# Performance work log

Measured on AMD Instinct MI355X. Metric: run time of the kernel, lower is better.

## Reference

```python
import jax, jax.numpy as jnp
import numpy as np

BATCH = 4096
IN_CAPS = 64
OUT_CAPS = 16
IN_DIM = 64
OUT_DIM = 64
NUM_ITER = 3
LN_EPS = 1e-5


def setup_inputs() -> dict:
    key = jax.random.key(0)
    ks = jax.random.split(key, 13)
    n = lambda k, s: jax.random.normal(k, s, dtype=jnp.float32)
    return {
        "x_inp": n(ks[0], (BATCH, IN_CAPS, IN_DIM)),
        "W_A": n(ks[1], (IN_CAPS, IN_DIM)),
        "B_A": n(ks[2], (IN_CAPS,)),
        "W_F1": n(ks[3], (IN_CAPS, IN_DIM, IN_DIM)),
        "W_F2": n(ks[4], (OUT_CAPS, IN_DIM, OUT_DIM)),
        "B_F2": n(ks[5], (OUT_CAPS, OUT_DIM)),
        "W_G1": n(ks[6], (OUT_DIM, OUT_DIM)),
        "W_G2": n(ks[7], (OUT_CAPS, OUT_DIM, IN_DIM)),
        "B_G2": n(ks[8], (OUT_CAPS, IN_DIM)),
        "ln_gamma": jnp.ones((OUT_DIM,), jnp.float32),
        "ln_beta": jnp.zeros((OUT_DIM,), jnp.float32),
        "W_S": n(ks[9], (IN_CAPS, OUT_CAPS, IN_DIM)),
        "B_S": n(ks[10], (IN_CAPS, OUT_CAPS)),
        "beta_use": n(ks[11], (IN_CAPS, OUT_CAPS)),
        "beta_ign": n(ks[12], (IN_CAPS, OUT_CAPS)),
    }


def _layer_norm(x, gamma, beta):
    mu = jnp.mean(x, axis=-1, keepdims=True)
    var = jnp.var(x, axis=-1, keepdims=True)  # biased, matches torch LayerNorm
    return (x - mu) * jax.lax.rsqrt(var + LN_EPS) * gamma + beta


def reference(x_inp, W_A, B_A, W_F1, W_F2, B_F2, W_G1, W_G2, B_G2,
              ln_gamma, ln_beta, W_S, B_S, beta_use, beta_ign):
    B = x_inp.shape[0]
    inv_sqrt = np.float32(1.0 / np.sqrt(IN_DIM))
    # activation logits per input capsule: [B, in_caps]
    a_e = jnp.einsum('bif,if->bi', x_inp, W_A) * inv_sqrt + B_A
    f_a_e = jax.nn.sigmoid(a_e)  # loop-invariant
    # temp_F is loop-invariant: [B, in_caps, in_dim]
    temp_F = jnp.einsum('bif,ifh->bih', x_inp, W_F1) * inv_sqrt
    R_em = jnp.full((B, IN_CAPS, OUT_CAPS), 1.0 / OUT_CAPS, dtype=x_inp.dtype)
    x_out = None
    for _ in range(NUM_ITER):
        D_use = f_a_e[:, :, None] * R_em                      # [B,i,m]
        D_ign = f_a_e[:, :, None] - D_use                     # [B,i,m]
        phi_em = beta_use * D_use - beta_ign * D_ign          # [B,i,m]
        temp_F_routed = phi_em.sum(axis=-1)[:, :, None] * temp_F  # [B,i,h]
        x_out = jnp.einsum('bih,mhd->bmd', temp_F_routed, W_F2) + B_F2  # [B,m,d]
        x_out_norm = _layer_norm(x_out, ln_gamma, ln_beta)
        temp_G = jnp.einsum('bmd,dh->bmh', x_out_norm, W_G1)  # [B,m,d]
        x_inp_hat = jnp.einsum('bmh,mhi->bmi', temp_G, W_G2) + B_G2  # [B,m,f]
        consistency = jnp.einsum('bif,bmf,imf->bim', x_inp, x_inp_hat, W_S) + B_S
        R_em = jax.nn.softmax(consistency, axis=-1)  # exp(log_softmax)
    return x_out
```

## Files before the change

kernel.cpp:

```cpp
#include <hip/hip_runtime.h>
#include <math.h>

#define IC 64
#define OC 16
#define DIM 64

__global__ void kSetup(const float* __restrict__ W_F2, const float* __restrict__ W_S,
                       const float* __restrict__ B_S, const float* __restrict__ bu,
                       const float* __restrict__ bi_, const float* __restrict__ W_G1,
                       const float* __restrict__ W_G2,
                       float* __restrict__ WF2t, float* __restrict__ WSt2,
                       float* __restrict__ WG12,
                       float* __restrict__ BSt, float* __restrict__ cb,
                       float* __restrict__ db, float* __restrict__ eb)
{
    int e = blockIdx.x * 256 + threadIdx.x;
    {
        int h = e >> 10, m = (e >> 6) & 15, d = e & 63;
        WF2t[e] = W_F2[((size_t)m * 64 + h) * 64 + d];
    }
    {
        int m = e >> 12, fo = (e >> 8) & 15, i = (e >> 2) & 63, fi = e & 3;
        WSt2[e] = W_S[((size_t)i * 16 + m) * 64 + fo * 4 + fi];
    }
    {
        int m = e >> 12, d = (e >> 6) & 63, f = e & 63;
        const float* g1 = W_G1 + d * 64;
        const float* g2 = W_G2 + (size_t)m * 4096 + f;
        float a = 0.f;
#pragma unroll 8
        for (int h = 0; h < 64; h++) a += g1[h] * g2[h * 64];
        WG12[e] = a;
    }
    if (e < 1024) {
        int m = e >> 6, i = e & 63;
        BSt[e] = B_S[i * 16 + m];
        cb[e] = bu[e] + bi_[e];
    }
    if (e < 64) {
        float sc = 0.f, sd = 0.f;
        for (int m = 0; m < 16; m++) {
            sc += bu[e * 16 + m] + bi_[e * 16 + m];
            sd += bi_[e * 16 + m];
        }
        db[e] = sd;
        eb[e] = sc * (1.0f / 16.0f) - sd;
    }
}

__global__ __launch_bounds__(256, 4)
void kT(const float* __restrict__ x, const float* __restrict__ W_A,
        const float* __restrict__ B_A, const float* __restrict__ eb,
        float* __restrict__ xq, float* __restrict__ fa, float* __restrict__ phi)
{
    __shared__ float Xs[2 * 64 * 65];
    const int t = threadIdx.x;
    const int blk = blockIdx.x;

    const float4* x4 = (const float4*)x;
#pragma unroll
    for (int s = 0; s < 8; s++) {
        int p = s * 256 + t;
        float4 v = x4[(size_t)blk * 2048 + p];
        int b = p >> 10, i = (p >> 4) & 63, fo = p & 15;
        float* row = &Xs[(b * 64 + i) * 65 + fo * 4];
        row[0] = v.x; row[1] = v.y; row[2] = v.z; row[3] = v.w;
    }
    __syncthreads();

    const int lane = t & 63, w = t >> 6;
#pragma unroll
    for (int s = 0; s < 8; s++) {
        int idx = s * 4 + w;
        int b = idx >> 4, fo = idx & 15;
        const float* row = &Xs[(b * 64 + lane) * 65 + fo * 4];
        ((float4*)xq)[((size_t)(blk * 2 + b) * 16 + fo) * 64 + lane] =
            make_float4(row[0], row[1], row[2], row[3]);
    }

    {
        int p = t >> 1, h = t & 1;
        int b = p >> 6, i = p & 63;
        const float* row = &Xs[(b * 64 + i) * 65 + h * 32];
        const float* wa = W_A + i * 64 + h * 32;
        float v = 0.f;
#pragma unroll
        for (int j = 0; j < 32; j++) v += row[j] * wa[j];
        v += __shfl_xor(v, 1);
        if (h == 0) {
            float ae = v * 0.125f + B_A[i];
            float fv = 1.0f / (1.0f + expf(-ae));
            size_t o = (size_t)(blk * 2 + b) * 64 + i;
            fa[o] = fv;
            phi[o] = fv * eb[i];
        }
    }
}

__global__ __launch_bounds__(256, 4)
void kA(const float* __restrict__ x, const float* __restrict__ W_F1,
        float* __restrict__ tF)
{
    __shared__ float XT[64][68];
    __shared__ float Ws[64][68];
    const int i = blockIdx.y;
    const int b0 = blockIdx.x * 64;
    const int t = threadIdx.x;
    const int bl = t >> 2, q = t & 3;

    {
        const float* src = x + ((size_t)(b0 + bl) * IC + i) * DIM + q * 4;
#pragma unroll
        for (int j4 = 0; j4 < 4; j4++) {
            float4 v = *(const float4*)(src + j4 * 16);
            int f = q * 4 + j4 * 16;
            XT[f + 0][bl] = v.x; XT[f + 1][bl] = v.y;
            XT[f + 2][bl] = v.z; XT[f + 3][bl] = v.w;
        }
        const float* wsrc = W_F1 + ((size_t)i * DIM + bl) * DIM + q * 4;
#pragma unroll
        for (int j4 = 0; j4 < 4; j4++)
            *(float4*)&Ws[bl][q * 4 + j4 * 16] = *(const float4*)(wsrc + j4 * 16);
    }
    __syncthreads();

    const int tr = t >> 4, tc = t & 15;
    float acc[4][4];
#pragma unroll
    for (int r = 0; r < 4; r++)
#pragma unroll
        for (int c = 0; c < 4; c++) acc[r][c] = 0.f;

#pragma unroll 8
    for (int k = 0; k < 64; k++) {
        float4 a = *(const float4*)&XT[k][tr * 4];
        float4 w = *(const float4*)&Ws[k][tc * 4];
        float ar[4] = {a.x, a.y, a.z, a.w};
#pragma unroll
        for (int r = 0; r < 4; r++) {
            acc[r][0] += ar[r] * w.x; acc[r][1] += ar[r] * w.y;
            acc[r][2] += ar[r] * w.z; acc[r][3] += ar[r] * w.w;
        }
    }
#pragma unroll
    for (int r = 0; r < 4; r++) {
        float4 o;
        o.x = acc[r][0] * 0.125f; o.y = acc[r][1] * 0.125f;
        o.z = acc[r][2] * 0.125f; o.w = acc[r][3] * 0.125f;
        *(float4*)&tF[((size_t)(b0 + tr * 4 + r) * IC + i) * DIM + tc * 4] = o;
    }
}

__global__ __launch_bounds__(256, 4)
void kS(const float* __restrict__ phi, const float* __restrict__ tF,
        float* __restrict__ s)
{
    __shared__ float ph[4 * 64];
    const int t = threadIdx.x;
    const int b0 = blockIdx.x * 4;
    ph[t] = phi[(size_t)b0 * 64 + t];
    __syncthreads();

    const int w = t >> 6, lane = t & 63;
    const int ig = lane >> 4, hq = lane & 15;
    const int b = b0 + w;
    const float4* tf4 = (const float4*)(tF + ((size_t)b * 64 + ig * 16) * 64) + hq;
    float4 a = make_float4(0.f, 0.f, 0.f, 0.f);
#pragma unroll
    for (int k = 0; k < 16; k++) {
        float p = ph[w * 64 + ig * 16 + k];
        float4 v = tf4[k * 16];
        a.x += p * v.x; a.y += p * v.y; a.z += p * v.z; a.w += p * v.w;
    }
#pragma unroll
    for (int k = 16; k <= 32; k <<= 1) {
        a.x += __shfl_xor(a.x, k); a.y += __shfl_xor(a.y, k);
        a.z += __shfl_xor(a.z, k); a.w += __shfl_xor(a.w, k);
    }
    if (ig == 0)
        ((float4*)(s + (size_t)b * 64))[hq] = a;
}

__global__ __launch_bounds__(256, 4)
void kXG(const float* __restrict__ s, const float* __restrict__ WF2t,
         const float* __restrict__ B_F2, const float* __restrict__ WG12,
         const float* __restrict__ B_G2,
         const float* __restrict__ gam, const float* __restrict__ bet,
         float* __restrict__ xhat, float* __restrict__ out, const int last)
{
    __shared__ float A[64][68];
    __shared__ float Wb[64][68];
    const int b0 = blockIdx.x * 64;
    const int m = blockIdx.y;
    const int t = threadIdx.x;
    const int bl = t >> 2, q = t & 3;
    const int tr = t >> 4, tc = t & 15;

    {
        const float* src = s + (size_t)(b0 + bl) * DIM + q * 4;
#pragma unroll
        for (int j4 = 0; j4 < 4; j4++) {
            float4 v = *(const float4*)(src + j4 * 16);
            int f = q * 4 + j4 * 16;
            A[f + 0][bl] = v.x; A[f + 1][bl] = v.y;
            A[f + 2][bl] = v.z; A[f + 3][bl] = v.w;
        }
        const float* wsrc = WF2t + ((size_t)bl * OC + m) * DIM + q * 4;
#pragma unroll
        for (int j4 = 0; j4 < 4; j4++)
            *(float4*)&Wb[bl][q * 4 + j4 * 16] = *(const float4*)(wsrc + j4 * 16);
    }
    __syncthreads();

    float acc[4][4];
#pragma unroll
    for (int r = 0; r < 4; r++)
#pragma unroll
        for (int c = 0; c < 4; c++) acc[r][c] = 0.f;
#pragma unroll 8
    for (int k = 0; k < 64; k++) {
        float4 a = *(const float4*)&A[k][tr * 4];
        float4 w = *(const float4*)&Wb[k][tc * 4];
        float ar[4] = {a.x, a.y, a.z, a.w};
#pragma unroll
        for (int r = 0; r < 4; r++) {
            acc[r][0] += ar[r] * w.x; acc[r][1] += ar[r] * w.y;
            acc[r][2] += ar[r] * w.z; acc[r][3] += ar[r] * w.w;
        }
    }
    {
        float4 bf = *(const float4*)&B_F2[m * DIM + tc * 4];
#pragma unroll
        for (int r = 0; r < 4; r++) {
            acc[r][0] += bf.x; acc[r][1] += bf.y;
            acc[r][2] += bf.z; acc[r][3] += bf.w;
        }
    }
    if (last) {
#pragma unroll
        for (int r = 0; r < 4; r++)
            *(float4*)&out[((size_t)(b0 + tr * 4 + r) * OC + m) * DIM + tc * 4] =
                make_float4(acc[r][0], acc[r][1], acc[r][2], acc[r][3]);
        return;
    }
    {
        float4 gv = *(const float4*)&gam[tc * 4];
        float4 bv = *(const float4*)&bet[tc * 4];
#pragma unroll
        for (int r = 0; r < 4; r++) {
            float sum = acc[r][0] + acc[r][1] + acc[r][2] + acc[r][3];
            float sq = acc[r][0] * acc[r][0] + acc[r][1] * acc[r][1] +
                       acc[r][2] * acc[r][2] + acc[r][3] * acc[r][3];
#pragma unroll
            for (int k = 1; k <= 8; k <<= 1) {
                sum += __shfl_xor(sum, k);
                sq  += __shfl_xor(sq, k);
            }
            float mu = sum * (1.0f / 64.0f);
            float var = sq * (1.0f / 64.0f) - mu * mu;
            float rs = 1.0f / sqrtf(var + 1e-5f);
            acc[r][0] = (acc[r][0] - mu) * rs * gv.x + bv.x;
            acc[r][1] = (acc[r][1] - mu) * rs * gv.y + bv.y;
            acc[r][2] = (acc[r][2] - mu) * rs * gv.z + bv.z;
            acc[r][3] = (acc[r][3] - mu) * rs * gv.w + bv.w;
        }
    }
    __syncthreads();
    {
#pragma unroll
        for (int r = 0; r < 4; r++)
#pragma unroll
            for (int c = 0; c < 4; c++)
                A[tc * 4 + c][tr * 4 + r] = acc[r][c];
        const float* wsrc = WG12 + ((size_t)m * DIM + bl) * DIM + q * 4;
#pragma unroll
        for (int j4 = 0; j4 < 4; j4++)
            *(float4*)&Wb[bl][q * 4 + j4 * 16] = *(const float4*)(wsrc + j4 * 16);
    }
    __syncthreads();

    float xh[4][4];
    {
        float4 bg = *(const float4*)&B_G2[m * DIM + tc * 4];
#pragma unroll
        for (int r = 0; r < 4; r++) {
            xh[r][0] = bg.x; xh[r][1] = bg.y; xh[r][2] = bg.z; xh[r][3] = bg.w;
        }
    }
#pragma unroll 8
    for (int k = 0; k < 64; k++) {
        float4 a = *(const float4*)&A[k][tr * 4];
        float4 w = *(const float4*)&Wb[k][tc * 4];
        float ar[4] = {a.x, a.y, a.z, a.w};
#pragma unroll
        for (int r = 0; r < 4; r++) {
            xh[r][0] += ar[r] * w.x; xh[r][1] += ar[r] * w.y;
            xh[r][2] += ar[r] * w.z; xh[r][3] += ar[r] * w.w;
        }
    }
#pragma unroll
    for (int r = 0; r < 4; r++)
        *(float4*)&xhat[((size_t)(b0 + tr * 4 + r) * OC + m) * DIM + tc * 4] =
            make_float4(xh[r][0], xh[r][1], xh[r][2], xh[r][3]);
}

__global__ __launch_bounds__(256, 4)
void kC(const float* __restrict__ xq, const float* __restrict__ xhat,
        const float* __restrict__ WSt2, const float* __restrict__ BSt,
        const float* __restrict__ cb, const float* __restrict__ db,
        const float* __restrict__ fa, float* __restrict__ phi)
{
    __shared__ float buf[4 * 64 * 17];
    const int b0 = blockIdx.x * 4;
    const int t = threadIdx.x;
    const int w = t >> 6, lane = t & 63;

    {
        const float4* src = (const float4*)(xhat + (size_t)b0 * OC * DIM);
        float4* dst = (float4*)buf;
#pragma unroll
        for (int j = 0; j < 4; j++) dst[t + j * 256] = src[t + j * 256];
    }
    __syncthreads();

    float acc[4][4];
#pragma unroll
    for (int k = 0; k < 4; k++) {
        float bs = BSt[(w * 4 + k) * IC + lane];
#pragma unroll
        for (int g = 0; g < 4; g++) acc[g][k] = bs;
    }

    const float4* xq4 = (const float4*)xq;
    for (int fc = 0; fc < 64; fc += 8) {
        const int fo = fc >> 2;
        float wreg[4][8];
#pragma unroll
        for (int k = 0; k < 4; k++) {
            int m = w * 4 + k;
#pragma unroll
            for (int q2 = 0; q2 < 2; q2++) {
                float4 v = *(const float4*)&WSt2[(((size_t)m * 16 + fo + q2) * IC + lane) * 4];
                wreg[k][q2 * 4 + 0] = v.x; wreg[k][q2 * 4 + 1] = v.y;
                wreg[k][q2 * 4 + 2] = v.z; wreg[k][q2 * 4 + 3] = v.w;
            }
        }
#pragma unroll
        for (int g = 0; g < 4; g++) {
            float xr[8];
#pragma unroll
            for (int q2 = 0; q2 < 2; q2++) {
                float4 v = xq4[((size_t)(b0 + g) * 16 + fo + q2) * 64 + lane];
                xr[q2 * 4 + 0] = v.x; xr[q2 * 4 + 1] = v.y;
                xr[q2 * 4 + 2] = v.z; xr[q2 * 4 + 3] = v.w;
            }
#pragma unroll
            for (int k = 0; k < 4; k++) {
                int m = w * 4 + k;
                const float* hp = &buf[(g * OC + m) * DIM + fc];
                float hr[8];
#pragma unroll
                for (int q2 = 0; q2 < 2; q2++) {
                    float4 v = *(const float4*)(hp + q2 * 4);
                    hr[q2 * 4 + 0] = v.x; hr[q2 * 4 + 1] = v.y;
                    hr[q2 * 4 + 2] = v.z; hr[q2 * 4 + 3] = v.w;
                }
#pragma unroll
                for (int ff = 0; ff < 8; ff++)
                    acc[g][k] += xr[ff] * hr[ff] * wreg[k][ff];
            }
        }
    }
    __syncthreads();
#pragma unroll
    for (int g = 0; g < 4; g++)
#pragma unroll
        for (int k = 0; k < 4; k++)
            buf[(g * IC + lane) * 17 + w * 4 + k] = acc[g][k];
    __syncthreads();

    {
        int g = t >> 6, i = t & 63;
        const float* row = &buf[(g * IC + i) * 17];
        float v[16], mx = -1e30f;
#pragma unroll
        for (int m = 0; m < OC; m++) { v[m] = row[m]; mx = fmaxf(mx, v[m]); }
        float sum = 0.f;
#pragma unroll
        for (int m = 0; m < OC; m++) { v[m] = expf(v[m] - mx); sum += v[m]; }
        float inv = 1.0f / sum;
        float a2 = 0.f;
#pragma unroll
        for (int m = 0; m < OC; m++) a2 += v[m] * inv * cb[i * OC + m];
        size_t bi = (size_t)(b0 + g) * IC + i;
        phi[bi] = fa[bi] * (a2 - db[i]);
    }
}

extern "C" void kernel_launch(void* const* d_in, const int* in_sizes, int n_in,
                              void* d_out, int out_size, void* d_ws, size_t ws_size,
                              hipStream_t stream)
{
    const float* x    = (const float*)d_in[0];
    const float* W_A  = (const float*)d_in[1];
    const float* B_A  = (const float*)d_in[2];
    const float* W_F1 = (const float*)d_in[3];
    const float* W_F2 = (const float*)d_in[4];
    const float* B_F2 = (const float*)d_in[5];
    const float* W_G1 = (const float*)d_in[6];
    const float* W_G2 = (const float*)d_in[7];
    const float* B_G2 = (const float*)d_in[8];
    const float* gam  = (const float*)d_in[9];
    const float* bet  = (const float*)d_in[10];
    const float* W_S  = (const float*)d_in[11];
    const float* B_S  = (const float*)d_in[12];
    const float* bu   = (const float*)d_in[13];
    const float* bi_  = (const float*)d_in[14];

    float* ws   = (float*)d_ws;
    float* tF   = ws;
    float* xq   = tF + 16777216;
    float* fa   = xq + 16777216;
    float* phi  = fa + 262144;
    float* s    = phi + 262144;
    float* xhat = s + 262144;
    float* WF2t = xhat + 4194304;
    float* WSt2 = WF2t + 65536;
    float* WG12 = WSt2 + 65536;
    float* BSt  = WG12 + 65536;
    float* cb   = BSt + 1024;
    float* db   = cb + 1024;
    float* eb   = db + 64;
    float* out  = (float*)d_out;

    kSetup<<<256, 256, 0, stream>>>(W_F2, W_S, B_S, bu, bi_, W_G1, W_G2,
                                    WF2t, WSt2, WG12, BSt, cb, db, eb);
    kT<<<2048, 256, 0, stream>>>(x, W_A, B_A, eb, xq, fa, phi);
    kA<<<dim3(64, 64), 256, 0, stream>>>(x, W_F1, tF);
    for (int it = 0; it < 3; ++it) {
        kS<<<1024, 256, 0, stream>>>(phi, tF, s);
        kXG<<<dim3(64, 16), 256, 0, stream>>>(s, WF2t, B_F2, WG12, B_G2,
                                              gam, bet, xhat, out, it == 2 ? 1 : 0);
        if (it < 2)
            kC<<<1024, 256, 0, stream>>>(xq, xhat, WSt2, BSt, cb, db, fa, phi);
    }
}
```

Before: 332.8 us.

## Use split-bf16 MFMA for temp_F GEMM and fuse phi-weighted reduction into kC

kA's per-capsule 64x64x64 GEMM now splits each fp32 operand into high and low bf16 halves and runs three bf16 MFMA products per tile (hi*hi, hi*lo, lo*hi), replacing the scalar FMA loop. Separately, the kS reduction that computes the phi-weighted sum over temp_F is folded into the tail of kC. This drops two kernel launches and the global phi round trip in the routing loop. The split-bf16 product gives close to fp32 accuracy but not exact, and kA's output stores are now scalar with a strided pattern instead of float4.

```diff
diff --git a/kernel.cpp b/kernel.cpp
--- a/kernel.cpp
+++ b/kernel.cpp
@@ -4,6 +4,18 @@
 #define IC 64
 #define OC 16
 #define DIM 64
+
+typedef __attribute__((ext_vector_type(8))) short bf16x8;
+typedef __attribute__((ext_vector_type(4))) float f32x4;
+
+__device__ __forceinline__ unsigned short f2bf(float f) {
+    unsigned int b = __float_as_uint(f);
+    b += 0x7fffu + ((b >> 16) & 1u);
+    return (unsigned short)(b >> 16);
+}
+__device__ __forceinline__ float bf2f(unsigned short h) {
+    return __uint_as_float(((unsigned int)h) << 16);
+}
 
 __global__ void kSetup(const float* __restrict__ W_F2, const float* __restrict__ W_S,
                        const float* __restrict__ B_S, const float* __restrict__ bu,
@@ -101,8 +113,8 @@
 void kA(const float* __restrict__ x, const float* __restrict__ W_F1,
         float* __restrict__ tF)
 {
-    __shared__ float XT[64][68];
-    __shared__ float Ws[64][68];
+    __shared__ unsigned short Ah[64][72], Al[64][72];
+    __shared__ unsigned short Bh[64][72], Bl[64][72];
     const int i = blockIdx.y;
     const int b0 = blockIdx.x * 64;
     const int t = threadIdx.x;
@@ -114,41 +126,64 @@
         for (int j4 = 0; j4 < 4; j4++) {
             float4 v = *(const float4*)(src + j4 * 16);
             int f = q * 4 + j4 * 16;
-            XT[f + 0][bl] = v.x; XT[f + 1][bl] = v.y;
-            XT[f + 2][bl] = v.z; XT[f + 3][bl] = v.w;
+            float vv[4] = {v.x, v.y, v.z, v.w};
+            ushort4 h4, l4;
+            unsigned short hh;
+            hh = f2bf(vv[0]); h4.x = hh; l4.x = f2bf(vv[0] - bf2f(hh));
+            hh = f2bf(vv[1]); h4.y = hh; l4.y = f2bf(vv[1] - bf2f(hh));
+            hh = f2bf(vv[2]); h4.z = hh; l4.z = f2bf(vv[2] - bf2f(hh));
+            hh = f2bf(vv[3]); h4.w = hh; l4.w = f2bf(vv[3] - bf2f(hh));
+            *(ushort4*)&Ah[bl][f] = h4;
+            *(ushort4*)&Al[bl][f] = l4;
         }
         const float* wsrc = W_F1 + ((size_t)i * DIM + bl) * DIM + q * 4;
 #pragma unroll
-        for (int j4 = 0; j4 < 4; j4++)
-            *(float4*)&Ws[bl][q * 4 + j4 * 16] = *(const float4*)(wsrc + j4 * 16);
-    }
-    __syncthreads();
-
-    const int tr = t >> 4, tc = t & 15;
-    float acc[4][4];
-#pragma unroll
-    for (int r = 0; r < 4; r++)
-#pragma unroll
-        for (int c = 0; c < 4; c++) acc[r][c] = 0.f;
-
-#pragma unroll 8
-    for (int k = 0; k < 64; k++) {
-        float4 a = *(const float4*)&XT[k][tr * 4];
-        float4 w = *(const float4*)&Ws[k][tc * 4];
-        float ar[4] = {a.x, a.y, a.z, a.w};
-#pragma unroll
-        for (int r = 0; r < 4; r++) {
-            acc[r][0] += ar[r] * w.x; acc[r][1] += ar[r] * w.y;
-            acc[r][2] += ar[r] * w.z; acc[r][3] += ar[r] * w.w;
-        }
-    }
-#pragma unroll
-    for (int r = 0; r < 4; r++) {
-        float4 o;
-        o.x = acc[r][0] * 0.125f; o.y = acc[r][1] * 0.125f;
-        o.z = acc[r][2] * 0.125f; o.w = acc[r][3] * 0.125f;
-        *(float4*)&tF[((size_t)(b0 + tr * 4 + r) * IC + i) * DIM + tc * 4] = o;
-    }
+        for (int j4 = 0; j4 < 4; j4++) {
+            float4 v = *(const float4*)(wsrc + j4 * 16);
+            int h0 = q * 4 + j4 * 16;
+            float vv[4] = {v.x, v.y, v.z, v.w};
+#pragma unroll
+            for (int c = 0; c < 4; c++) {
+                unsigned short hh = f2bf(vv[c]);
+                Bh[h0 + c][bl] = hh;
+                Bl[h0 + c][bl] = f2bf(vv[c] - bf2f(hh));
+            }
+        }
+    }
+    __syncthreads();
+
+    const int w = t >> 6, lane = t & 63;
+    const int fm = lane & 15, fq = lane >> 4;
+    const int r0 = w * 16;
+    f32x4 acc[4];
+#pragma unroll
+    for (int nt = 0; nt < 4; nt++) {
+        acc[nt][0] = 0.f; acc[nt][1] = 0.f; acc[nt][2] = 0.f; acc[nt][3] = 0.f;
+    }
+
+#pragma unroll
+    for (int ks = 0; ks < 2; ks++) {
+        const int kk = ks * 32 + fq * 8;
+        bf16x8 ah = *(const bf16x8*)&Ah[r0 + fm][kk];
+        bf16x8 al = *(const bf16x8*)&Al[r0 + fm][kk];
+#pragma unroll
+        for (int nt = 0; nt < 4; nt++) {
+            bf16x8 bh = *(const bf16x8*)&Bh[nt * 16 + fm][kk];
+            bf16x8 bl2 = *(const bf16x8*)&Bl[nt * 16 + fm][kk];
+            acc[nt] = __builtin_amdgcn_mfma_f32_16x16x32_bf16(ah, bh, acc[nt], 0, 0, 0);
+            acc[nt] = __builtin_amdgcn_mfma_f32_16x16x32_bf16(ah, bl2, acc[nt], 0, 0, 0);
+            acc[nt] = __builtin_amdgcn_mfma_f32_16x16x32_bf16(al, bh, acc[nt], 0, 0, 0);
+        }
+    }
+
+#pragma unroll
+    for (int nt = 0; nt < 4; nt++)
+#pragma unroll
+        for (int j = 0; j < 4; j++) {
+            int row = r0 + fq * 4 + j;
+            int col = nt * 16 + fm;
+            tF[((size_t)(b0 + row) * IC + i) * DIM + col] = acc[nt][j] * 0.125f;
+        }
 }
 
 __global__ __launch_bounds__(256, 4)
@@ -308,9 +343,11 @@
 void kC(const float* __restrict__ xq, const float* __restrict__ xhat,
         const float* __restrict__ WSt2, const float* __restrict__ BSt,
         const float* __restrict__ cb, const float* __restrict__ db,
-        const float* __restrict__ fa, float* __restrict__ phi)
+        const float* __restrict__ fa, const float* __restrict__ tF,
+        float* __restrict__ s)
 {
     __shared__ float buf[4 * 64 * 17];
+    __shared__ float phs[4][64];
     const int b0 = blockIdx.x * 4;
     const int t = threadIdx.x;
     const int w = t >> 6, lane = t & 63;
@@ -392,8 +429,28 @@
         float a2 = 0.f;
 #pragma unroll
         for (int m = 0; m < OC; m++) a2 += v[m] * inv * cb[i * OC + m];
-        size_t bi = (size_t)(b0 + g) * IC + i;
-        phi[bi] = fa[bi] * (a2 - db[i]);
+        phs[g][i] = fa[(size_t)(b0 + g) * IC + i] * (a2 - db[i]);
+    }
+    __syncthreads();
+
+    {
+        const int ig = lane >> 4, hq = lane & 15;
+        const int b = b0 + w;
+        const float4* tf4 = (const float4*)(tF + ((size_t)b * 64 + ig * 16) * 64) + hq;
+        float4 a = make_float4(0.f, 0.f, 0.f, 0.f);
+#pragma unroll
+        for (int k = 0; k < 16; k++) {
+            float p = phs[w][ig * 16 + k];
+            float4 v = tf4[k * 16];
+            a.x += p * v.x; a.y += p * v.y; a.z += p * v.z; a.w += p * v.w;
+        }
+#pragma unroll
+        for (int k = 16; k <= 32; k <<= 1) {
+            a.x += __shfl_xor(a.x, k); a.y += __shfl_xor(a.y, k);
+            a.z += __shfl_xor(a.z, k); a.w += __shfl_xor(a.w, k);
+        }
+        if (ig == 0)
+            ((float4*)(s + (size_t)b * 64))[hq] = a;
     }
 }
 
@@ -437,11 +494,11 @@
                                     WF2t, WSt2, WG12, BSt, cb, db, eb);
     kT<<<2048, 256, 0, stream>>>(x, W_A, B_A, eb, xq, fa, phi);
     kA<<<dim3(64, 64), 256, 0, stream>>>(x, W_F1, tF);
+    kS<<<1024, 256, 0, stream>>>(phi, tF, s);
     for (int it = 0; it < 3; ++it) {
-        kS<<<1024, 256, 0, stream>>>(phi, tF, s);
         kXG<<<dim3(64, 16), 256, 0, stream>>>(s, WF2t, B_F2, WG12, B_G2,
                                               gam, bet, xhat, out, it == 2 ? 1 : 0);
         if (it < 2)
-            kC<<<1024, 256, 0, stream>>>(xq, xhat, WSt2, BSt, cb, db, fa, phi);
-    }
-}
+            kC<<<1024, 256, 0, stream>>>(xq, xhat, WSt2, BSt, cb, db, fa, tF, s);
+    }
+}
```

After: 307.7 us. 7.5% less time.
